# Kernel optimization log

Hardware: AMD Instinct MI355X
Metric: run time of the kernel (lower is better)

Reference implementation:

```python
import jax, jax.numpy as jnp
import numpy as np

DATA_WIDTH = 8  # fixed-point data width; bitstream length L = 2**DATA_WIDTH


def gen_bitstream(x, rng, data_width):
    """Vectorized GenBitstreamGroup.

    For each element x: if x == 0 -> Zero flag set, all-zero bitstream.
    Otherwise normalize |x| into [0.5, 1) via leftShift (number of left
    shifts), then unary-encode the normalized value against the RNG
    sequence: bit_t = 1 iff rng[t] < floor(norm * L).
    Returns (bits [..., L], leftShift [...], zero [...]).
    """
    L = rng.shape[0]
    zero = (x == 0)
    ax = jnp.abs(x)
    safe = jnp.where(zero, jnp.float32(1.0), ax)
    # leftShift: smallest s >= 0 with |x| * 2**s in [0.5, 1)
    s = jnp.clip(jnp.floor(-jnp.log2(safe)), 0.0, jnp.float32(data_width))
    norm = ax * jnp.exp2(s)                       # normalized magnitude in [0.5, 1]
    thresh = jnp.floor(norm * L)                  # integer threshold in [0, L]
    bits = (rng.astype(jnp.float32)[None, None, :] < thresh[:, :, None]).astype(jnp.float32)
    bits = jnp.where(zero[:, :, None], jnp.float32(0.0), bits)
    return bits, s, zero


def setup_inputs() -> dict:
    key = jax.random.key(0)
    k1, k2 = jax.random.split(key)
    M, K, N = 256, 256, 256
    L = 2 ** DATA_WIDTH
    tensor_1 = jax.random.uniform(k1, (M, K), dtype=jnp.float32)
    tensor_2 = jax.random.uniform(k2, (K, N), dtype=jnp.float32)
    rngSeq = jnp.arange(L, dtype=jnp.int32)
    return {"tensor_1": tensor_1, "tensor_2": tensor_2, "rngSeq": rngSeq}


def reference(tensor_1, tensor_2, rngSeq):
    L = rngSeq.shape[0]
    ascending = jnp.arange(L, dtype=jnp.int32)  # module's ascendingSeq for tensor_2
    b1, s1, z1 = gen_bitstream(tensor_1, rngSeq, DATA_WIDTH)      # [M,K,L]
    b2, s2, z2 = gen_bitstream(tensor_2, ascending, DATA_WIDTH)   # [K,N,L]
    # BitstreamMUL: AND the two bitstreams, popcount, rescale by bitstream
    # length and undo the normalization left-shifts.
    count = jnp.einsum('mkl,knl->mnk', b1, b2)                    # [M,N,K] popcounts
    scale = jnp.exp2(-(s1[:, None, :] + s2.T[None, :, :])) / L    # [M,N,K]
    valid = ((~z1)[:, None, :] & (~z2).T[None, :, :]).astype(jnp.float32)
    sgn = jnp.sign(tensor_1)[:, None, :] * jnp.sign(tensor_2).T[None, :, :]
    sc = count * scale * valid * sgn                              # per-k SC products
    return sc.sum(axis=-1)                                        # [M,N] result
```

## Files before the change

kernel.cpp:

```cpp
#include <hip/hip_runtime.h>


constexpr int DIM = 256;
constexpr int MK  = DIM * DIM;

__device__ inline unsigned pack_sc(float v) {
    unsigned ub = __float_as_uint(v);
    unsigned ax = ub & 0x7fffffffu;
    if (ax == 0u) return 0u;
    int B        = (int)(ax >> 23);
    unsigned mnt = ax & 0x7fffffu;
    int s = 126 - B + (mnt == 0u ? 1 : 0);
    s = s < 0 ? 0 : (s > 8 ? 8 : s);
    float scaled = __uint_as_float(ax) * __uint_as_float((unsigned)(127 + s + 8) << 23);
    unsigned t = (unsigned)scaled;
    t = t > 256u ? 256u : t;
    unsigned fb = (ub & 0x80000000u) | ((unsigned)(127 - s) << 23);
    return (fb & 0xFFFF0000u) | t;
}

__global__ __launch_bounds__(256) void precomp2_kernel(
    const float* __restrict__ x2, unsigned* __restrict__ P2)
{
    int i = blockIdx.x * 256 + threadIdx.x;
    P2[i] = pack_sc(x2[i]);
}

__global__ __launch_bounds__(1024) void scgemm_kernel(
    const float* __restrict__ x1, const unsigned* __restrict__ P2,
    float* __restrict__ out)
{
    __shared__ unsigned sT[DIM];
    __shared__ float    sF[DIM];
    __shared__ float    part[4][DIM];

    const int tid = threadIdx.x;
    const int m   = blockIdx.x;
    const int n   = tid & (DIM - 1);
    const int kc  = tid >> 8;

    if (tid < DIM) {
        unsigned p = pack_sc(x1[m * DIM + tid]);
        sT[tid] = p & 0xFFFFu;
        sF[tid] = __uint_as_float(p & 0xFFFF0000u);
    }
    __syncthreads();

    float acc = 0.0f;
    const int kbase = kc * 64;
    #pragma unroll 8
    for (int kk = 0; kk < 64; ++kk) {
        const int k  = kbase + kk;
        unsigned u2  = P2[k * DIM + n];
        unsigned t2  = u2 & 0xFFFFu;
        float    f2  = __uint_as_float(u2 & 0xFFFF0000u);
        unsigned c   = min(sT[k], t2);
        acc = fmaf((float)c, sF[k] * f2, acc);
    }
    part[kc][n] = acc;
    __syncthreads();
    if (tid < DIM) {
        float r = part[0][tid] + part[1][tid] + part[2][tid] + part[3][tid];
        out[m * DIM + tid] = r * (1.0f / 256.0f);
    }
}

extern "C" void kernel_launch(void* const* d_in, const int* in_sizes, int n_in,
                              void* d_out, int out_size, void* d_ws, size_t ws_size,
                              hipStream_t stream)
{
    const float* x1 = (const float*)d_in[0];
    const float* x2 = (const float*)d_in[1];

    unsigned* P2  = (unsigned*)d_ws;
    float*    out = (float*)d_out;

    hipLaunchKernelGGL(precomp2_kernel, dim3(MK / 256), dim3(256), 0, stream, x2, P2);
    hipLaunchKernelGGL(scgemm_kernel, dim3(DIM), dim3(1024), 0, stream, x1, P2, out);
}
```

Before: 62.46 us.

## Fuse tensor_2 preprocessing into GEMM kernel with float4 loads and float math

Removes the separate precompute kernel and workspace pass by recomputing the per-element threshold and scale of tensor_2 inside the main kernel. Each thread now loads float4 vectors covering four n columns, splits K into 16 chunks, and reduces partials over 16 shared-memory rows. Packing uses float frexp/ldexp instead of integer bit tricks. It saves one launch and the workspace round trip, but every block redoes the tensor_2 packing (256x redundant ALU work).

```diff
diff --git a/kernel.cpp b/kernel.cpp
--- a/kernel.cpp
+++ b/kernel.cpp
@@ -2,65 +2,65 @@
 
 
 constexpr int DIM = 256;
-constexpr int MK  = DIM * DIM;
 
-__device__ inline unsigned pack_sc(float v) {
-    unsigned ub = __float_as_uint(v);
-    unsigned ax = ub & 0x7fffffffu;
-    if (ax == 0u) return 0u;
-    int B        = (int)(ax >> 23);
-    unsigned mnt = ax & 0x7fffffu;
-    int s = 126 - B + (mnt == 0u ? 1 : 0);
+__device__ inline void pack2(float v, float& tf, float& af) {
+    float ax = fabsf(v);
+    int   E;
+    float fm = frexpf(ax, &E);
+    int s = (fm == 0.5f ? 1 : 0) - E;
     s = s < 0 ? 0 : (s > 8 ? 8 : s);
-    float scaled = __uint_as_float(ax) * __uint_as_float((unsigned)(127 + s + 8) << 23);
-    unsigned t = (unsigned)scaled;
-    t = t > 256u ? 256u : t;
-    unsigned fb = (ub & 0x80000000u) | ((unsigned)(127 - s) << 23);
-    return (fb & 0xFFFF0000u) | t;
+    tf = floorf(ldexpf(ax, s + 8));
+    tf = fminf(tf, 256.0f);
+    af = ldexpf(copysignf(1.0f, v), -s);
 }
 
-__global__ __launch_bounds__(256) void precomp2_kernel(
-    const float* __restrict__ x2, unsigned* __restrict__ P2)
-{
-    int i = blockIdx.x * 256 + threadIdx.x;
-    P2[i] = pack_sc(x2[i]);
-}
-
-__global__ __launch_bounds__(1024) void scgemm_kernel(
-    const float* __restrict__ x1, const unsigned* __restrict__ P2,
+__global__ __launch_bounds__(1024) void scgemm_fused(
+    const float* __restrict__ x1, const float* __restrict__ x2,
     float* __restrict__ out)
 {
-    __shared__ unsigned sT[DIM];
-    __shared__ float    sF[DIM];
-    __shared__ float    part[4][DIM];
+    __shared__ float sT[DIM];
+    __shared__ float sF[DIM];
+    __shared__ float part[16][DIM];
 
     const int tid = threadIdx.x;
     const int m   = blockIdx.x;
-    const int n   = tid & (DIM - 1);
-    const int kc  = tid >> 8;
 
     if (tid < DIM) {
-        unsigned p = pack_sc(x1[m * DIM + tid]);
-        sT[tid] = p & 0xFFFFu;
-        sF[tid] = __uint_as_float(p & 0xFFFF0000u);
+        float tf, af;
+        pack2(x1[m * DIM + tid], tf, af);
+        sT[tid] = tf;
+        sF[tid] = af;
     }
     __syncthreads();
 
-    float acc = 0.0f;
-    const int kbase = kc * 64;
-    #pragma unroll 8
-    for (int kk = 0; kk < 64; ++kk) {
-        const int k  = kbase + kk;
-        unsigned u2  = P2[k * DIM + n];
-        unsigned t2  = u2 & 0xFFFFu;
-        float    f2  = __uint_as_float(u2 & 0xFFFF0000u);
-        unsigned c   = min(sT[k], t2);
-        acc = fmaf((float)c, sF[k] * f2, acc);
+    const int n0 = (tid & 63) * 4;
+    const int kc = tid >> 6;
+    const float4* __restrict__ x2v = (const float4*)x2;
+
+    float acc0 = 0.f, acc1 = 0.f, acc2 = 0.f, acc3 = 0.f;
+    #pragma unroll 4
+    for (int kk = 0; kk < 16; ++kk) {
+        const int k = kc * 16 + kk;
+        float4 v = x2v[(k * DIM + n0) >> 2];
+        float t0, a0, t1, a1, t2, a2, t3, a3;
+        pack2(v.x, t0, a0);
+        pack2(v.y, t1, a1);
+        pack2(v.z, t2, a2);
+        pack2(v.w, t3, a3);
+        const float T1 = sT[k];
+        const float F1 = sF[k];
+        acc0 = fmaf(fminf(T1, t0), F1 * a0, acc0);
+        acc1 = fmaf(fminf(T1, t1), F1 * a1, acc1);
+        acc2 = fmaf(fminf(T1, t2), F1 * a2, acc2);
+        acc3 = fmaf(fminf(T1, t3), F1 * a3, acc3);
     }
-    part[kc][n] = acc;
+    *(float4*)&part[kc][n0] = make_float4(acc0, acc1, acc2, acc3);
     __syncthreads();
+
     if (tid < DIM) {
-        float r = part[0][tid] + part[1][tid] + part[2][tid] + part[3][tid];
+        float r = 0.f;
+        #pragma unroll
+        for (int c = 0; c < 16; ++c) r += part[c][tid];
         out[m * DIM + tid] = r * (1.0f / 256.0f);
     }
 }
@@ -69,12 +69,9 @@
                               void* d_out, int out_size, void* d_ws, size_t ws_size,
                               hipStream_t stream)
 {
-    const float* x1 = (const float*)d_in[0];
-    const float* x2 = (const float*)d_in[1];
+    const float* x1  = (const float*)d_in[0];
+    const float* x2  = (const float*)d_in[1];
+    float* out = (float*)d_out;
 
-    unsigned* P2  = (unsigned*)d_ws;
-    float*    out = (float*)d_out;
-
-    hipLaunchKernelGGL(precomp2_kernel, dim3(MK / 256), dim3(256), 0, stream, x2, P2);
-    hipLaunchKernelGGL(scgemm_kernel, dim3(DIM), dim3(1024), 0, stream, x1, P2, out);
+    hipLaunchKernelGGL(scgemm_fused, dim3(DIM), dim3(1024), 0, stream, x1, x2, out);
 }
```

Result: slower. 65.57 us (+5.0%).
